# Optimization experiments

Hardware: AMD Instinct MI355X
Metric: run time of the kernel (lower is better)

The kernel has to match this reference:

```python
import jax, jax.numpy as jnp
import numpy as np

B, N, M = 4, 2048, 2048
DIM, DIM_KEYS, DIM_OUT = 512, 512, 512
HEADS, DIM_HEAD = 8, 64
INNER = HEADS * DIM_HEAD


def setup_inputs() -> dict:
    key = jax.random.key(0)
    ks = jax.random.split(key, 9)
    x = jax.random.normal(ks[0], (B, N, DIM), dtype=jnp.float32)
    context = jax.random.normal(ks[1], (B, M, DIM_KEYS), dtype=jnp.float32)
    mask = jax.random.randint(ks[2], (B, N), 0, 2).astype(bool)
    context_mask = jax.random.randint(ks[3], (B, M), 0, 2).astype(bool)
    Wq = jax.random.normal(ks[4], (DIM, INNER), dtype=jnp.float32) * 0.02
    Wkv = jax.random.normal(ks[5], (DIM_KEYS, 2 * INNER), dtype=jnp.float32) * 0.02
    Wo = jax.random.normal(ks[6], (INNER, DIM_OUT), dtype=jnp.float32) * 0.02
    bo = jnp.zeros((DIM_OUT,), dtype=jnp.float32)
    null_key = jax.random.normal(ks[7], (DIM_HEAD,), dtype=jnp.float32)
    null_value = jax.random.normal(ks[8], (DIM_HEAD,), dtype=jnp.float32)
    return {"x": x, "context": context, "mask": mask, "context_mask": context_mask,
            "Wq": Wq, "Wkv": Wkv, "Wo": Wo, "bo": bo,
            "null_key": null_key, "null_value": null_value}


def reference(x, context, mask, context_mask, Wq, Wkv, Wo, bo, null_key, null_value):
    b, n, _ = x.shape
    m = context.shape[1]
    h, dh = HEADS, DIM_HEAD
    scale = dh ** -0.5

    # projections -> [b, h, n, dh]
    q = (x @ Wq).reshape(b, n, h, dh).transpose(0, 2, 1, 3)
    kv = context @ Wkv  # [b, m, 2*inner]
    k, v = jnp.split(kv, 2, axis=-1)
    k = k.reshape(b, m, h, dh).transpose(0, 2, 1, 3)
    v = v.reshape(b, m, h, dh).transpose(0, 2, 1, 3)

    # prepend null key/value token -> j = m + 1
    nk = jnp.broadcast_to(null_key, (b, h, 1, dh))
    nv = jnp.broadcast_to(null_value, (b, h, 1, dh))
    k = jnp.concatenate([nk, k], axis=2)
    v = jnp.concatenate([nv, v], axis=2)

    # qk activation (tanh) BEFORE the dot product
    q = jnp.tanh(q)
    k = jnp.tanh(k)

    sim = jnp.einsum('bhid,bhjd->bhij', q, k) * scale  # [b,h,n,m+1]

    # null token is always attendable -> pad context mask with True
    cm = jnp.pad(context_mask, ((0, 0), (1, 0)), constant_values=True)
    full_mask = mask[:, None, :, None] & cm[:, None, None, :]
    neg = -jnp.finfo(sim.dtype).max
    sim = jnp.where(full_mask, sim, neg)

    attn = jax.nn.softmax(sim, axis=-1)
    out = jnp.einsum('bhij,bhjd->bhid', attn, v)
    out = out.transpose(0, 2, 1, 3).reshape(b, n, h * dh)
    return out @ Wo + bo
```

## Files before the change

### kernel.cpp

```cpp
#include <hip/hip_runtime.h>
#include <math.h>

#define BB 4
#define NN 2048
#define MM 2048
#define HEADS 8
#define DH 64

typedef _Float16 f16;
typedef _Float16 f16x4 __attribute__((ext_vector_type(4)));
typedef _Float16 f16x8 __attribute__((ext_vector_type(8)));
typedef float f32x4 __attribute__((ext_vector_type(4)));
typedef unsigned short ushort;

#define LOG2E 1.44269504088896f
#define QSCALE (0.125f * LOG2E)

#if __has_builtin(__builtin_amdgcn_exp2f)
#define EXP2(x) __builtin_amdgcn_exp2f(x)
#else
#define EXP2(x) exp2f(x)
#endif

__device__ __forceinline__ f16x4 pk4(float a, float b, float c, float d) {
#if __has_builtin(__builtin_amdgcn_cvt_pkrtz)
    auto t0 = __builtin_amdgcn_cvt_pkrtz(a, b);
    auto t1 = __builtin_amdgcn_cvt_pkrtz(c, d);
    f16x4 r;
    r[0] = t0[0]; r[1] = t0[1]; r[2] = t1[0]; r[3] = t1[1];
    return r;
#else
    f16x4 r = {(f16)a, (f16)b, (f16)c, (f16)d};
    return r;
#endif
}

__device__ __forceinline__ void gl16(const void* g, void* l) {
    __builtin_amdgcn_global_load_lds(
        (const __attribute__((address_space(1))) unsigned int*)g,
        (__attribute__((address_space(3))) unsigned int*)l, 16, 0, 0);
}

__global__ void wprep_k(const float* __restrict__ Wq, const float* __restrict__ Wkv,
                        const float* __restrict__ Wo,
                        f16* __restrict__ wq16, f16* __restrict__ wkv16,
                        f16* __restrict__ woh, f16* __restrict__ wol)
{
    __shared__ f16 S0[64 * 36], S1[64 * 36];
    const int tid = threadIdx.x;
    const int bid = blockIdx.x;
    const int K = 512;
    const float* W; int N; f16* T16; f16 *Th, *Tl; int id;
    if (bid < 128)      { W = Wq;  N = 512;  T16 = wq16;  Th = 0; Tl = 0; id = bid; }
    else if (bid < 384) { W = Wkv; N = 1024; T16 = wkv16; Th = 0; Tl = 0; id = bid - 128; }
    else                { W = Wo;  N = 512;  T16 = 0; Th = woh; Tl = wol; id = bid - 384; }
    const int k0 = (id & 15) * 32, n0 = (id >> 4) * 64;
    const int kr = tid >> 3, nc = (tid & 7) * 8;
    float4 v0 = *(const float4*)(W + (size_t)(k0 + kr) * N + n0 + nc);
    float4 v1 = *(const float4*)(W + (size_t)(k0 + kr) * N + n0 + nc + 4);
    float e[8] = {v0.x, v0.y, v0.z, v0.w, v1.x, v1.y, v1.z, v1.w};
    const int n = tid >> 2, kc = (tid & 3) * 8;
    if (T16) {
#pragma unroll
        for (int j = 0; j < 8; j++) S0[(nc + j) * 36 + kr] = (f16)e[j];
        __syncthreads();
        *(uint4*)(T16 + (size_t)(n0 + n) * K + k0 + kc) = *(const uint4*)(S0 + n * 36 + kc);
    } else {
#pragma unroll
        for (int j = 0; j < 8; j++) {
            f16 h = (f16)e[j];
            S0[(nc + j) * 36 + kr] = h;
            S1[(nc + j) * 36 + kr] = (f16)(e[j] - (float)h);
        }
        __syncthreads();
        *(uint4*)(Th + (size_t)(n0 + n) * K + k0 + kc) = *(const uint4*)(S0 + n * 36 + kc);
        *(uint4*)(Tl + (size_t)(n0 + n) * K + k0 + kc) = *(const uint4*)(S1 + n * 36 + kc);
    }
}

__launch_bounds__(256)
__global__ void proj_k(const float* __restrict__ x, const float* __restrict__ ctx,
                       const f16* __restrict__ wq16, const f16* __restrict__ wkv16,
                       f16* __restrict__ qws, f16* __restrict__ kws, f16* __restrict__ vt)
{
    __shared__ f16 sA[128 * 36];
    __shared__ f16 sB[128 * 36];

    const int tid  = threadIdx.x;
    const int wave = tid >> 6, lane = tid & 63;
    const int l15  = lane & 15, quad = lane >> 4;
    const int by = blockIdx.y;
    const int isQ = (by < 4);
    const float* A = isQ ? x : ctx;
    const f16* Bt  = isQ ? wq16 : wkv16;
    const int c0 = (isQ ? by : by - 4) * 128;
    const size_t r0 = (size_t)blockIdx.x * 128;
    const int K = 512;

    const int ar = tid >> 1;
    const int ac = (tid & 1) * 16;

    f32x4 acc[2][8] = {};

    for (int k0 = 0; k0 < K; k0 += 32) {
        const float* ap = A + (r0 + ar) * K + k0 + ac;
        float4 a0 = *(const float4*)(ap + 0);
        float4 a1 = *(const float4*)(ap + 4);
        float4 a2 = *(const float4*)(ap + 8);
        float4 a3 = *(const float4*)(ap + 12);
        uint4 bv0 = *(const uint4*)(Bt + (size_t)(c0 + ar) * K + k0 + ac);
        uint4 bv1 = *(const uint4*)(Bt + (size_t)(c0 + ar) * K + k0 + ac + 8);
        f16x8 pa0, pa1;
        pa0[0] = (f16)a0.x; pa0[1] = (f16)a0.y; pa0[2] = (f16)a0.z; pa0[3] = (f16)a0.w;
        pa0[4] = (f16)a1.x; pa0[5] = (f16)a1.y; pa0[6] = (f16)a1.z; pa0[7] = (f16)a1.w;
        pa1[0] = (f16)a2.x; pa1[1] = (f16)a2.y; pa1[2] = (f16)a2.z; pa1[3] = (f16)a2.w;
        pa1[4] = (f16)a3.x; pa1[5] = (f16)a3.y; pa1[6] = (f16)a3.z; pa1[7] = (f16)a3.w;
        __syncthreads();
        *(f16x8*)(sA + ar * 36 + ac)     = pa0;
        *(f16x8*)(sA + ar * 36 + ac + 8) = pa1;
        *(uint4*)(sB + ar * 36 + ac)     = bv0;
        *(uint4*)(sB + ar * 36 + ac + 8) = bv1;
        __syncthreads();

        f16x8 a[2];
#pragma unroll
        for (int rt = 0; rt < 2; rt++)
            a[rt] = *(const f16x8*)(sA + (wave * 32 + rt * 16 + l15) * 36 + quad * 8);
#pragma unroll
        for (int half = 0; half < 2; half++) {
            f16x8 b[4];
#pragma unroll
            for (int c = 0; c < 4; c++)
                b[c] = *(const f16x8*)(sB + ((half * 4 + c) * 16 + l15) * 36 + quad * 8);
#pragma unroll
            for (int rt = 0; rt < 2; rt++)
#pragma unroll
                for (int c = 0; c < 4; c++)
                    acc[rt][half * 4 + c] = __builtin_amdgcn_mfma_f32_16x16x32_f16(
                        a[rt], b[c], acc[rt][half * 4 + c], 0, 0, 0);
        }
    }

    const int b    = (int)(r0 >> 11);
    const int rloc = ((int)(r0 & 2047)) + wave * 32;

#pragma unroll
    for (int rt = 0; rt < 2; rt++)
#pragma unroll
        for (int ct = 0; ct < 8; ct++) {
            const int col = c0 + ct * 16 + l15;
            if (isQ || col < 512) {
                const int h = (col >> 6) & 7;
                const int d = col & 63;
                f16* dst = isQ ? qws : kws;
                const float sc = isQ ? QSCALE : 1.0f;
#pragma unroll
                for (int reg = 0; reg < 4; reg++) {
                    const int nn = rloc + rt * 16 + quad * 4 + reg;
                    dst[(((size_t)b * 8 + h) * 2048 + nn) * 64 + d] =
                        (f16)(tanhf(acc[rt][ct][reg]) * sc);
                }
            } else {
                const int c = col - 512;
                const int h = c >> 6;
                const int d = c & 63;
                const int m0 = rloc + rt * 16 + quad * 4;
                f16x4 pk;
#pragma unroll
                for (int reg = 0; reg < 4; reg++) pk[reg] = (f16)acc[rt][ct][reg];
                *(f16x4*)(vt + (((size_t)b * 8 + h) * 64 + d) * 2048 + m0) = pk;
            }
        }
}

__launch_bounds__(256, 4)
__global__ void attn_k(const f16* __restrict__ qws, const f16* __restrict__ kws,
                       const f16* __restrict__ vtws,
                       const int* __restrict__ mask, const int* __restrict__ cmask,
                       const float* __restrict__ nk, const float* __restrict__ nv,
                       f16* __restrict__ Opf, float* __restrict__ lp)
{
    __shared__ __align__(16) char smem[32768];

    const int tid  = threadIdx.x;
    const int wave = tid >> 6, lane = tid & 63;
    const int l15  = lane & 15, quad = lane >> 4;
    const int bh = blockIdx.x, b = bh >> 3, h = bh & 7;
    const int q0 = blockIdx.y * 128 + wave * 32;
    const int jh = blockIdx.z;
    const int jbeg = jh << 9, jend = jbeg + 512;

    const f16* kg0 = kws + (size_t)bh * MM * DH;
    const f16* vg0 = vtws + (size_t)bh * DH * MM;

    const int lrow = lane >> 3;
    const int lsw  = ((lane & 7) ^ lrow) << 4;
    const char* kP = (const char*)kg0 + (size_t)(jbeg + wave * 16 + lrow) * 128 + lsw;
    const char* vP = (const char*)vg0 + (size_t)(wave * 16 + lrow) * 4096
                   + (size_t)jbeg * 2 + lsw;
    char* kD = smem + wave * 2048;
    char* vD = smem + 8192 + wave * 2048;

    gl16(kP,         kD);
    gl16(kP + 1024,  kD + 1024);
    gl16(vP,         vD);
    gl16(vP + 32768, vD + 1024);
    kP += 8192; vP += 128;

    f16x8 qf[2][2];
    const f16* qbase = qws + ((size_t)bh * NN + q0) * DH;
#pragma unroll
    for (int rt = 0; rt < 2; rt++)
#pragma unroll
        for (int ks = 0; ks < 2; ks++)
            qf[rt][ks] = *(const f16x8*)(qbase + (rt * 16 + l15) * DH + ks * 32 + quad * 8);

    int rowOk[2];
#pragma unroll
    for (int rt = 0; rt < 2; rt++)
        rowOk[rt] = mask[(size_t)b * NN + q0 + rt * 16 + l15];

    float pnull[2] = {0.0f, 0.0f};
    if (jh == 0) {
        float pn[2] = {0.f, 0.f};
#pragma unroll
        for (int ks = 0; ks < 2; ks++)
#pragma unroll
            for (int t = 0; t < 8; t++) {
                const float nkt = tanhf(nk[ks * 32 + quad * 8 + t]);
                pn[0] += (float)qf[0][ks][t] * nkt;
                pn[1] += (float)qf[1][ks][t] * nkt;
            }
#pragma unroll
        for (int rt = 0; rt < 2; rt++) {
            pn[rt] += __shfl_xor(pn[rt], 16);
            pn[rt] += __shfl_xor(pn[rt], 32);
            pnull[rt] = rowOk[rt] ? EXP2(pn[rt]) : 1.0f;
        }
    }
    float negsel[2];
#pragma unroll
    for (int rt = 0; rt < 2; rt++) {
        negsel[rt] = rowOk[rt] ? -1.0e30f : 0.0f;
        if (!rowOk[rt]) {
            const f16x8 zz = {(f16)0, (f16)0, (f16)0, (f16)0, (f16)0, (f16)0, (f16)0, (f16)0};
            qf[rt][0] = zz; qf[rt][1] = zz;
        }
    }

    f32x4 acc[2][4];
    f32x4 accl[2];
#pragma unroll
    for (int rt = 0; rt < 2; rt++)
#pragma unroll
        for (int reg = 0; reg < 4; reg++) {
            const float pr = __shfl(pnull[rt], quad * 4 + reg, 16);
            accl[rt][reg] = pr;
#pragma unroll
            for (int ds = 0; ds < 4; ds++)
                acc[rt][ds][reg] = pr * nv[ds * 16 + l15];
        }

    const f16x4 vone = {(f16)1, (f16)1, (f16)1, (f16)1};
    const int kxor = l15 & 7;

    __syncthreads();

    int buf = 0;
    for (int jc = jbeg; jc < jend; jc += 64) {
        int4 cmv[4];
#pragma unroll
        for (int jj = 0; jj < 4; jj++)
            cmv[jj] = *(const int4*)(cmask + (size_t)b * MM + jc + jj * 16 + quad * 4);

        if (jc + 64 < jend) {
            const int bo = (buf ^ 1) << 14;
            gl16(kP,         kD + bo);
            gl16(kP + 1024,  kD + bo + 1024);
            gl16(vP,         vD + bo);
            gl16(vP + 32768, vD + bo + 1024);
            kP += 8192; vP += 128;
        }

        const char* sKb = smem + (buf << 14);
        const char* sVb = sKb + 8192;

        f32x4 st[2][4];
#pragma unroll
        for (int rt = 0; rt < 2; rt++)
#pragma unroll
            for (int jj = 0; jj < 4; jj++) {
                st[rt][jj][0] = cmv[jj].x ? 0.0f : negsel[rt];
                st[rt][jj][1] = cmv[jj].y ? 0.0f : negsel[rt];
                st[rt][jj][2] = cmv[jj].z ? 0.0f : negsel[rt];
                st[rt][jj][3] = cmv[jj].w ? 0.0f : negsel[rt];
            }

#pragma unroll
        for (int ks = 0; ks < 2; ks++) {
            f16x8 kb[4];
#pragma unroll
            for (int jj = 0; jj < 4; jj++)
                kb[jj] = *(const f16x8*)(sKb + (jj * 16 + l15) * 128
                                             + (((ks * 4 + quad) ^ kxor) << 4));
#pragma unroll
            for (int rt = 0; rt < 2; rt++)
#pragma unroll
                for (int jj = 0; jj < 4; jj++)
                    st[rt][jj] = __builtin_amdgcn_mfma_f32_16x16x32_f16(
                        kb[jj], qf[rt][ks], st[rt][jj], 0, 0, 0);
        }

        f16x4 pa[2][4];
#pragma unroll
        for (int rt = 0; rt < 2; rt++)
#pragma unroll
            for (int jj = 0; jj < 4; jj++)
                pa[rt][jj] = pk4(EXP2(st[rt][jj][0]), EXP2(st[rt][jj][1]),
                                 EXP2(st[rt][jj][2]), EXP2(st[rt][jj][3]));

#pragma unroll
        for (int jj = 0; jj < 4; jj++) {
            f16x4 vb[4];
#pragma unroll
            for (int ds = 0; ds < 4; ds++)
                vb[ds] = *(const f16x4*)(sVb + (ds * 16 + l15) * 128
                                             + (((jj * 2 + (quad >> 1)) ^ kxor) << 4)
                                             + ((quad & 1) << 3));
#pragma unroll
            for (int rt = 0; rt < 2; rt++) {
#pragma unroll
                for (int ds = 0; ds < 4; ds++)
                    acc[rt][ds] = __builtin_amdgcn_mfma_f32_16x16x16f16(
                        pa[rt][jj], vb[ds], acc[rt][ds], 0, 0, 0);
                accl[rt] = __builtin_amdgcn_mfma_f32_16x16x16f16(
                    pa[rt][jj], vone, accl[rt], 0, 0, 0);
            }
        }

        __syncthreads();
        buf ^= 1;
    }

#pragma unroll
    for (int rt = 0; rt < 2; rt++) {
        float inv[4];
#pragma unroll
        for (int reg = 0; reg < 4; reg++)
            inv[reg] = 1.0f / fmaxf(accl[rt][reg], 1e-35f);
#pragma unroll
        for (int ds = 0; ds < 4; ds++)
#pragma unroll
            for (int reg = 0; reg < 4; reg++) {
                const int r = q0 + rt * 16 + quad * 4 + reg;
                Opf[((size_t)jh * 8192 + b * 2048 + r) * 512 + h * 64 + ds * 16 + l15] =
                    (f16)(acc[rt][ds][reg] * inv[reg]);
            }
    }
    if (l15 == 0) {
#pragma unroll
        for (int rt = 0; rt < 2; rt++)
#pragma unroll
            for (int reg = 0; reg < 4; reg++)
                lp[((size_t)jh * 32 + bh) * 2048 + q0 + rt * 16 + quad * 4 + reg] =
                    accl[rt][reg];
    }
}

__global__ void merge_k(const f16* __restrict__ Opf, const float* __restrict__ lp,
                        f16* __restrict__ of16)
{
    const int i = blockIdx.x * 256 + threadIdx.x;
    const int row = i >> 7;
    const int c4  = i & 127;
    const int b = row >> 11, n = row & 2047, h = c4 >> 4;
    float w[4], den = 0.f;
#pragma unroll
    for (int jh = 0; jh < 4; jh++) {
        w[jh] = lp[((size_t)jh * 32 + b * 8 + h) * 2048 + n];
        den += w[jh];
    }
    const float inv = 1.0f / den;
    float v0 = 0, v1 = 0, v2 = 0, v3 = 0;
#pragma unroll
    for (int jh = 0; jh < 4; jh++) {
        f16x4 o = *(const f16x4*)(Opf + ((size_t)jh * 8192 + row) * 512 + c4 * 4);
        v0 += (float)o[0] * w[jh];
        v1 += (float)o[1] * w[jh];
        v2 += (float)o[2] * w[jh];
        v3 += (float)o[3] * w[jh];
    }
    f16x4 r = pk4(v0 * inv, v1 * inv, v2 * inv, v3 * inv);
    *(f16x4*)(of16 + (size_t)row * 512 + c4 * 4) = r;
}

__launch_bounds__(256)
__global__ void mgemm2(const f16* __restrict__ A, const f16* __restrict__ Bh,
                       const f16* __restrict__ Bl,
                       float* __restrict__ o32, const float* __restrict__ bias,
                       int K)
{
    __shared__ f16 sA[128 * 36];
    __shared__ f16 sBh[64 * 36], sBl[64 * 36];

    const int tid  = threadIdx.x;
    const int wave = tid >> 6, lane = tid & 63;
    const int l15  = lane & 15, quad = lane >> 4;
    const size_t r0 = (size_t)blockIdx.x * 128;
    const int c0 = blockIdx.y * 64;

    const int sr = tid >> 2;
    const int sc = (tid & 3) * 8;

    f32x4 acc[2][4] = {};

    for (int k0 = 0; k0 < K; k0 += 32) {
        uint4 a0 = *(const uint4*)(A + (r0 + sr) * K + k0 + sc);
        uint4 a1 = *(const uint4*)(A + (r0 + 64 + sr) * K + k0 + sc);
        uint4 bh = *(const uint4*)(Bh + (size_t)(c0 + sr) * K + k0 + sc);
        uint4 bl = *(const uint4*)(Bl + (size_t)(c0 + sr) * K + k0 + sc);
        __syncthreads();
        *(uint4*)(sA + sr * 36 + sc)        = a0;
        *(uint4*)(sA + (64 + sr) * 36 + sc) = a1;
        *(uint4*)(sBh + sr * 36 + sc)       = bh;
        *(uint4*)(sBl + sr * 36 + sc)       = bl;
        __syncthreads();

        f16x8 a[2], b_h[4], b_l[4];
#pragma unroll
        for (int rt = 0; rt < 2; rt++)
            a[rt] = *(const f16x8*)(sA + (wave * 32 + rt * 16 + l15) * 36 + quad * 8);
#pragma unroll
        for (int ct = 0; ct < 4; ct++) {
            b_h[ct] = *(const f16x8*)(sBh + (ct * 16 + l15) * 36 + quad * 8);
            b_l[ct] = *(const f16x8*)(sBl + (ct * 16 + l15) * 36 + quad * 8);
        }
#pragma unroll
        for (int rt = 0; rt < 2; rt++)
#pragma unroll
            for (int ct = 0; ct < 4; ct++) {
                acc[rt][ct] = __builtin_amdgcn_mfma_f32_16x16x32_f16(a[rt], b_h[ct], acc[rt][ct], 0, 0, 0);
                acc[rt][ct] = __builtin_amdgcn_mfma_f32_16x16x32_f16(a[rt], b_l[ct], acc[rt][ct], 0, 0, 0);
            }
    }

#pragma unroll
    for (int rt = 0; rt < 2; rt++)
#pragma unroll
        for (int ct = 0; ct < 4; ct++) {
            const int col = c0 + ct * 16 + l15;
            const float bv = bias[col];
#pragma unroll
            for (int reg = 0; reg < 4; reg++) {
                const size_t row = r0 + wave * 32 + rt * 16 + quad * 4 + reg;
                o32[row * 512 + col] = acc[rt][ct][reg] + bv;
            }
        }
}

extern "C" void kernel_launch(void* const* d_in, const int* in_sizes, int n_in,
                              void* d_out, int out_size, void* d_ws, size_t ws_size,
                              hipStream_t stream)
{
    const float* x    = (const float*)d_in[0];
    const float* ctx  = (const float*)d_in[1];
    const int*   mask = (const int*)d_in[2];
    const int*   cmsk = (const int*)d_in[3];
    const float* Wq   = (const float*)d_in[4];
    const float* Wkv  = (const float*)d_in[5];
    const float* Wo   = (const float*)d_in[6];
    const float* bo   = (const float*)d_in[7];
    const float* nk   = (const float*)d_in[8];
    const float* nv   = (const float*)d_in[9];
    float* out = (float*)d_out;

    const size_t S = (size_t)BB * HEADS * NN * DH;

    f16* qws = (f16*)d_ws;
    f16* kws = qws + S;
    f16* vt  = kws + S;
    f16* wq16  = vt + S;
    f16* wkv16 = wq16 + 512 * 512;
    f16* woh = wkv16 + 512 * 1024;
    f16* wol = woh + 512 * 512;
    float* lp = (float*)(wol + 512 * 512);
    f16* Opf = (f16*)(lp + 4 * 32 * 2048);
    f16* of16 = qws;

    wprep_k<<<512, 256, 0, stream>>>(Wq, Wkv, Wo, wq16, wkv16, woh, wol);
    proj_k<<<dim3(64, 12), 256, 0, stream>>>(x, ctx, wq16, wkv16, qws, kws, vt);
    attn_k<<<dim3(32, 16, 4), 256, 0, stream>>>(qws, kws, vt, mask, cmsk, nk, nv, Opf, lp);
    merge_k<<<4096, 256, 0, stream>>>(Opf, lp, of16);
    mgemm2<<<dim3(64, 8), 256, 0, stream>>>(of16, woh, wol, out, bo, 512);
}
```

Before: 201.1 us.

## Pre-convert activations to fp16, precompute mask bias, unroll attention double-buffer loop

A new xprep kernel converts x and context to fp16 once, so the projection GEMM loads half-width A tiles instead of converting fp32 inside every K-step. The context mask becomes a float additive bias in wprep, and attention applies it by multiplying with a per-row float instead of branching on integer selects. The attention loop is manually unrolled into ping-pong tiles with constant buffer offsets, explicit vmcnt waits, a raw barrier and sched_barriers. The extra conversion kernel adds a full read and write of both activations and one more launch, which may cost more than the per-tile conversion work it replaces.

```diff
diff --git a/kernel.cpp b/kernel.cpp
--- a/kernel.cpp
+++ b/kernel.cpp
@@ -42,13 +42,27 @@
 }
 
 __global__ void wprep_k(const float* __restrict__ Wq, const float* __restrict__ Wkv,
-                        const float* __restrict__ Wo,
+                        const float* __restrict__ Wo, const int* __restrict__ cmask,
                         f16* __restrict__ wq16, f16* __restrict__ wkv16,
-                        f16* __restrict__ woh, f16* __restrict__ wol)
+                        f16* __restrict__ woh, f16* __restrict__ wol,
+                        float* __restrict__ cbias)
 {
     __shared__ f16 S0[64 * 36], S1[64 * 36];
     const int tid = threadIdx.x;
     const int bid = blockIdx.x;
+    if (bid >= 512) {
+        const int bb = bid - 512, j0 = tid * 8;
+        int4 m0 = *(const int4*)(cmask + (size_t)bb * MM + j0);
+        int4 m1 = *(const int4*)(cmask + (size_t)bb * MM + j0 + 4);
+        float4 o0, o1;
+        o0.x = m0.x ? 0.f : -1e30f; o0.y = m0.y ? 0.f : -1e30f;
+        o0.z = m0.z ? 0.f : -1e30f; o0.w = m0.w ? 0.f : -1e30f;
+        o1.x = m1.x ? 0.f : -1e30f; o1.y = m1.y ? 0.f : -1e30f;
+        o1.z = m1.z ? 0.f : -1e30f; o1.w = m1.w ? 0.f : -1e30f;
+        *(float4*)(cbias + (size_t)bb * MM + j0)     = o0;
+        *(float4*)(cbias + (size_t)bb * MM + j0 + 4) = o1;
+        return;
+    }
     const int K = 512;
     const float* W; int N; f16* T16; f16 *Th, *Tl; int id;
     if (bid < 128)      { W = Wq;  N = 512;  T16 = wq16;  Th = 0; Tl = 0; id = bid; }
@@ -78,8 +92,23 @@
     }
 }
 
+__global__ void xprep_k(const float* __restrict__ x, const float* __restrict__ ctx,
+                        f16* __restrict__ xf, f16* __restrict__ cf)
+{
+    const size_t S = (size_t)BB * NN * 512;
+    const size_t i = ((size_t)blockIdx.x * 256 + threadIdx.x) * 8;
+    const float* src = (i < S) ? x + i : ctx + (i - S);
+    f16* dst         = (i < S) ? xf + i : cf + (i - S);
+    float4 v0 = *(const float4*)(src);
+    float4 v1 = *(const float4*)(src + 4);
+    f16x8 o;
+    o[0] = (f16)v0.x; o[1] = (f16)v0.y; o[2] = (f16)v0.z; o[3] = (f16)v0.w;
+    o[4] = (f16)v1.x; o[5] = (f16)v1.y; o[6] = (f16)v1.z; o[7] = (f16)v1.w;
+    *(f16x8*)dst = o;
+}
+
 __launch_bounds__(256)
-__global__ void proj_k(const float* __restrict__ x, const float* __restrict__ ctx,
+__global__ void proj_k(const f16* __restrict__ xf, const f16* __restrict__ cf,
                        const f16* __restrict__ wq16, const f16* __restrict__ wkv16,
                        f16* __restrict__ qws, f16* __restrict__ kws, f16* __restrict__ vt)
 {
@@ -91,7 +120,7 @@
     const int l15  = lane & 15, quad = lane >> 4;
     const int by = blockIdx.y;
     const int isQ = (by < 4);
-    const float* A = isQ ? x : ctx;
+    const f16* A16 = isQ ? xf : cf;
     const f16* Bt  = isQ ? wq16 : wkv16;
     const int c0 = (isQ ? by : by - 4) * 128;
     const size_t r0 = (size_t)blockIdx.x * 128;
@@ -103,21 +132,13 @@
     f32x4 acc[2][8] = {};
 
     for (int k0 = 0; k0 < K; k0 += 32) {
-        const float* ap = A + (r0 + ar) * K + k0 + ac;
-        float4 a0 = *(const float4*)(ap + 0);
-        float4 a1 = *(const float4*)(ap + 4);
-        float4 a2 = *(const float4*)(ap + 8);
-        float4 a3 = *(const float4*)(ap + 12);
+        uint4 av0 = *(const uint4*)(A16 + (r0 + ar) * K + k0 + ac);
+        uint4 av1 = *(const uint4*)(A16 + (r0 + ar) * K + k0 + ac + 8);
         uint4 bv0 = *(const uint4*)(Bt + (size_t)(c0 + ar) * K + k0 + ac);
         uint4 bv1 = *(const uint4*)(Bt + (size_t)(c0 + ar) * K + k0 + ac + 8);
-        f16x8 pa0, pa1;
-        pa0[0] = (f16)a0.x; pa0[1] = (f16)a0.y; pa0[2] = (f16)a0.z; pa0[3] = (f16)a0.w;
-        pa0[4] = (f16)a1.x; pa0[5] = (f16)a1.y; pa0[6] = (f16)a1.z; pa0[7] = (f16)a1.w;
-        pa1[0] = (f16)a2.x; pa1[1] = (f16)a2.y; pa1[2] = (f16)a2.z; pa1[3] = (f16)a2.w;
-        pa1[4] = (f16)a3.x; pa1[5] = (f16)a3.y; pa1[6] = (f16)a3.z; pa1[7] = (f16)a3.w;
         __syncthreads();
-        *(f16x8*)(sA + ar * 36 + ac)     = pa0;
-        *(f16x8*)(sA + ar * 36 + ac + 8) = pa1;
+        *(uint4*)(sA + ar * 36 + ac)     = av0;
+        *(uint4*)(sA + ar * 36 + ac + 8) = av1;
         *(uint4*)(sB + ar * 36 + ac)     = bv0;
         *(uint4*)(sB + ar * 36 + ac + 8) = bv1;
         __syncthreads();
@@ -176,7 +197,7 @@
 __launch_bounds__(256, 4)
 __global__ void attn_k(const f16* __restrict__ qws, const f16* __restrict__ kws,
                        const f16* __restrict__ vtws,
-                       const int* __restrict__ mask, const int* __restrict__ cmask,
+                       const int* __restrict__ mask, const float* __restrict__ cbias,
                        const float* __restrict__ nk, const float* __restrict__ nv,
                        f16* __restrict__ Opf, float* __restrict__ lp)
 {
@@ -188,7 +209,7 @@
     const int bh = blockIdx.x, b = bh >> 3, h = bh & 7;
     const int q0 = blockIdx.y * 128 + wave * 32;
     const int jh = blockIdx.z;
-    const int jbeg = jh << 9, jend = jbeg + 512;
+    const int jbeg = jh << 9;
 
     const f16* kg0 = kws + (size_t)bh * MM * DH;
     const f16* vg0 = vtws + (size_t)bh * DH * MM;
@@ -238,10 +259,10 @@
             pnull[rt] = rowOk[rt] ? EXP2(pn[rt]) : 1.0f;
         }
     }
-    float negsel[2];
+    float rowOkf[2];
 #pragma unroll
     for (int rt = 0; rt < 2; rt++) {
-        negsel[rt] = rowOk[rt] ? -1.0e30f : 0.0f;
+        rowOkf[rt] = rowOk[rt] ? 1.0f : 0.0f;
         if (!rowOk[rt]) {
             const f16x8 zz = {(f16)0, (f16)0, (f16)0, (f16)0, (f16)0, (f16)0, (f16)0, (f16)0};
             qf[rt][0] = zz; qf[rt][1] = zz;
@@ -263,84 +284,85 @@
 
     const f16x4 vone = {(f16)1, (f16)1, (f16)1, (f16)1};
     const int kxor = l15 & 7;
-
-    __syncthreads();
-
-    int buf = 0;
-    for (int jc = jbeg; jc < jend; jc += 64) {
-        int4 cmv[4];
-#pragma unroll
-        for (int jj = 0; jj < 4; jj++)
-            cmv[jj] = *(const int4*)(cmask + (size_t)b * MM + jc + jj * 16 + quad * 4);
-
-        if (jc + 64 < jend) {
-            const int bo = (buf ^ 1) << 14;
-            gl16(kP,         kD + bo);
-            gl16(kP + 1024,  kD + bo + 1024);
-            gl16(vP,         vD + bo);
-            gl16(vP + 32768, vD + bo + 1024);
-            kP += 8192; vP += 128;
-        }
-
-        const char* sKb = smem + (buf << 14);
-        const char* sVb = sKb + 8192;
-
-        f32x4 st[2][4];
-#pragma unroll
-        for (int rt = 0; rt < 2; rt++)
-#pragma unroll
-            for (int jj = 0; jj < 4; jj++) {
-                st[rt][jj][0] = cmv[jj].x ? 0.0f : negsel[rt];
-                st[rt][jj][1] = cmv[jj].y ? 0.0f : negsel[rt];
-                st[rt][jj][2] = cmv[jj].z ? 0.0f : negsel[rt];
-                st[rt][jj][3] = cmv[jj].w ? 0.0f : negsel[rt];
-            }
-
-#pragma unroll
-        for (int ks = 0; ks < 2; ks++) {
-            f16x8 kb[4];
-#pragma unroll
-            for (int jj = 0; jj < 4; jj++)
-                kb[jj] = *(const f16x8*)(sKb + (jj * 16 + l15) * 128
-                                             + (((ks * 4 + quad) ^ kxor) << 4));
-#pragma unroll
-            for (int rt = 0; rt < 2; rt++)
-#pragma unroll
-                for (int jj = 0; jj < 4; jj++)
-                    st[rt][jj] = __builtin_amdgcn_mfma_f32_16x16x32_f16(
-                        kb[jj], qf[rt][ks], st[rt][jj], 0, 0, 0);
-        }
-
-        f16x4 pa[2][4];
-#pragma unroll
-        for (int rt = 0; rt < 2; rt++)
-#pragma unroll
-            for (int jj = 0; jj < 4; jj++)
-                pa[rt][jj] = pk4(EXP2(st[rt][jj][0]), EXP2(st[rt][jj][1]),
-                                 EXP2(st[rt][jj][2]), EXP2(st[rt][jj][3]));
-
-#pragma unroll
-        for (int jj = 0; jj < 4; jj++) {
-            f16x4 vb[4];
-#pragma unroll
-            for (int ds = 0; ds < 4; ds++)
-                vb[ds] = *(const f16x4*)(sVb + (ds * 16 + l15) * 128
-                                             + (((jj * 2 + (quad >> 1)) ^ kxor) << 4)
-                                             + ((quad & 1) << 3));
-#pragma unroll
-            for (int rt = 0; rt < 2; rt++) {
-#pragma unroll
-                for (int ds = 0; ds < 4; ds++)
-                    acc[rt][ds] = __builtin_amdgcn_mfma_f32_16x16x16f16(
-                        pa[rt][jj], vb[ds], acc[rt][ds], 0, 0, 0);
-                accl[rt] = __builtin_amdgcn_mfma_f32_16x16x16f16(
-                    pa[rt][jj], vone, accl[rt], 0, 0, 0);
-            }
-        }
-
-        __syncthreads();
-        buf ^= 1;
-    }
+    const float* cbb = cbias + (size_t)b * MM;
+
+#define ATTN_TILE(BUF, NXT, JC, PF)                                           \
+  {                                                                           \
+    asm volatile("s_waitcnt vmcnt(0)" ::: "memory");                          \
+    __builtin_amdgcn_s_barrier();                                             \
+    __builtin_amdgcn_sched_barrier(0);                                        \
+    float4 cbv[4];                                                            \
+    _Pragma("unroll")                                                         \
+    for (int jj = 0; jj < 4; jj++)                                            \
+      cbv[jj] = *(const float4*)(cbb + (JC) + jj * 16 + quad * 4);            \
+    __builtin_amdgcn_sched_barrier(0);                                        \
+    if (PF) {                                                                 \
+      gl16(kP,         kD + (NXT));                                           \
+      gl16(kP + 1024,  kD + (NXT) + 1024);                                    \
+      gl16(vP,         vD + (NXT));                                           \
+      gl16(vP + 32768, vD + (NXT) + 1024);                                    \
+      kP += 8192; vP += 128;                                                  \
+    }                                                                         \
+    __builtin_amdgcn_sched_barrier(0);                                        \
+    const char* sKb = smem + (BUF);                                           \
+    const char* sVb = smem + (BUF) + 8192;                                    \
+    f32x4 st[2][4];                                                           \
+    _Pragma("unroll")                                                         \
+    for (int rt = 0; rt < 2; rt++)                                            \
+      _Pragma("unroll")                                                       \
+      for (int jj = 0; jj < 4; jj++)                                          \
+        _Pragma("unroll")                                                     \
+        for (int reg = 0; reg < 4; reg++)                                     \
+          st[rt][jj][reg] = cbv[jj][reg] * rowOkf[rt];                        \
+    _Pragma("unroll")                                                         \
+    for (int ks = 0; ks < 2; ks++) {                                          \
+      f16x8 kb[4];                                                            \
+      _Pragma("unroll")                                                       \
+      for (int jj = 0; jj < 4; jj++)                                          \
+        kb[jj] = *(const f16x8*)(sKb + (jj * 16 + l15) * 128                  \
+                                     + (((ks * 4 + quad) ^ kxor) << 4));      \
+      _Pragma("unroll")                                                       \
+      for (int rt = 0; rt < 2; rt++)                                          \
+        _Pragma("unroll")                                                     \
+        for (int jj = 0; jj < 4; jj++)                                        \
+          st[rt][jj] = __builtin_amdgcn_mfma_f32_16x16x32_f16(                \
+              kb[jj], qf[rt][ks], st[rt][jj], 0, 0, 0);                       \
+    }                                                                         \
+    f16x4 pa[2][4];                                                           \
+    _Pragma("unroll")                                                         \
+    for (int rt = 0; rt < 2; rt++)                                            \
+      _Pragma("unroll")                                                       \
+      for (int jj = 0; jj < 4; jj++)                                          \
+        pa[rt][jj] = pk4(EXP2(st[rt][jj][0]), EXP2(st[rt][jj][1]),            \
+                         EXP2(st[rt][jj][2]), EXP2(st[rt][jj][3]));           \
+    _Pragma("unroll")                                                         \
+    for (int jj = 0; jj < 4; jj++) {                                          \
+      f16x4 vb[4];                                                            \
+      _Pragma("unroll")                                                       \
+      for (int ds = 0; ds < 4; ds++)                                          \
+        vb[ds] = *(const f16x4*)(sVb + (ds * 16 + l15) * 128                  \
+                                     + (((jj * 2 + (quad >> 1)) ^ kxor) << 4) \
+                                     + ((quad & 1) << 3));                    \
+      _Pragma("unroll")                                                       \
+      for (int rt = 0; rt < 2; rt++) {                                        \
+        _Pragma("unroll")                                                     \
+        for (int ds = 0; ds < 4; ds++)                                        \
+          acc[rt][ds] = __builtin_amdgcn_mfma_f32_16x16x16f16(                \
+              pa[rt][jj], vb[ds], acc[rt][ds], 0, 0, 0);                      \
+        accl[rt] = __builtin_amdgcn_mfma_f32_16x16x16f16(                     \
+            pa[rt][jj], vone, accl[rt], 0, 0, 0);                             \
+      }                                                                       \
+    }                                                                         \
+  }
+
+    int jc = jbeg;
+    for (int it = 0; it < 4; it++) {
+        ATTN_TILE(0,     16384, jc, 1);
+        jc += 64;
+        ATTN_TILE(16384, 0,     jc, it < 3);
+        jc += 64;
+    }
+#undef ATTN_TILE
 
 #pragma unroll
     for (int rt = 0; rt < 2; rt++) {
@@ -486,10 +508,14 @@
     float* lp = (float*)(wol + 512 * 512);
     f16* Opf = (f16*)(lp + 4 * 32 * 2048);
     f16* of16 = qws;
-
-    wprep_k<<<512, 256, 0, stream>>>(Wq, Wkv, Wo, wq16, wkv16, woh, wol);
-    proj_k<<<dim3(64, 12), 256, 0, stream>>>(x, ctx, wq16, wkv16, qws, kws, vt);
-    attn_k<<<dim3(32, 16, 4), 256, 0, stream>>>(qws, kws, vt, mask, cmsk, nk, nv, Opf, lp);
+    f16* xf16 = Opf;
+    f16* cf16 = xf16 + (size_t)BB * NN * 512;
+    float* cbias = (float*)(Opf + (size_t)4 * 8192 * 512);
+
+    wprep_k<<<516, 256, 0, stream>>>(Wq, Wkv, Wo, cmsk, wq16, wkv16, woh, wol, cbias);
+    xprep_k<<<4096, 256, 0, stream>>>(x, ctx, xf16, cf16);
+    proj_k<<<dim3(64, 12), 256, 0, stream>>>(xf16, cf16, wq16, wkv16, qws, kws, vt);
+    attn_k<<<dim3(32, 16, 4), 256, 0, stream>>>(qws, kws, vt, mask, cbias, nk, nv, Opf, lp);
     merge_k<<<4096, 256, 0, stream>>>(Opf, lp, of16);
     mgemm2<<<dim3(64, 8), 256, 0, stream>>>(of16, woh, wol, out, bo, 512);
 }
```

After: 205.8 us. +2.3%, slower.

## Double-buffer projection and output GEMMs with async global-to-LDS loads

Applied to the files above, without the earlier changes.

Adds a pre-pass kernel that converts x and context to fp16 so the projection GEMM can stream fp16 tiles. Both the projection GEMM and the output GEMM now use double-buffered LDS filled by direct global-to-LDS loads (gl16) with an XOR swizzle instead of padding. The output GEMM tile widens from 64 to 128 columns. This targets global-load latency and register staging in the GEMM main loops, at the cost of an extra kernel launch and an extra round trip through memory for the converted activations.

```diff
diff --git a/kernel.cpp b/kernel.cpp
--- a/kernel.cpp
+++ b/kernel.cpp
@@ -78,60 +78,79 @@
     }
 }
 
-__launch_bounds__(256)
-__global__ void proj_k(const float* __restrict__ x, const float* __restrict__ ctx,
+__global__ void xprep_k(const float* __restrict__ x, const float* __restrict__ ctx,
+                        f16* __restrict__ xf, f16* __restrict__ cf)
+{
+    const size_t S = (size_t)BB * NN * 512;
+    const size_t i = ((size_t)blockIdx.x * 256 + threadIdx.x) * 8;
+    const float* src = (i < S) ? x + i : ctx + (i - S);
+    f16* dst         = (i < S) ? xf + i : cf + (i - S);
+    float4 v0 = *(const float4*)(src);
+    float4 v1 = *(const float4*)(src + 4);
+    f16x8 o;
+    o[0] = (f16)v0.x; o[1] = (f16)v0.y; o[2] = (f16)v0.z; o[3] = (f16)v0.w;
+    o[4] = (f16)v1.x; o[5] = (f16)v1.y; o[6] = (f16)v1.z; o[7] = (f16)v1.w;
+    *(f16x8*)dst = o;
+}
+
+__launch_bounds__(256, 3)
+__global__ void proj_k(const f16* __restrict__ xf, const f16* __restrict__ cf,
                        const f16* __restrict__ wq16, const f16* __restrict__ wkv16,
                        f16* __restrict__ qws, f16* __restrict__ kws, f16* __restrict__ vt)
 {
-    __shared__ f16 sA[128 * 36];
-    __shared__ f16 sB[128 * 36];
+    __shared__ __align__(16) char smem[32768];
 
     const int tid  = threadIdx.x;
     const int wave = tid >> 6, lane = tid & 63;
     const int l15  = lane & 15, quad = lane >> 4;
     const int by = blockIdx.y;
     const int isQ = (by < 4);
-    const float* A = isQ ? x : ctx;
+    const f16* A16 = isQ ? xf : cf;
     const f16* Bt  = isQ ? wq16 : wkv16;
     const int c0 = (isQ ? by : by - 4) * 128;
     const size_t r0 = (size_t)blockIdx.x * 128;
     const int K = 512;
 
-    const int ar = tid >> 1;
-    const int ac = (tid & 1) * 16;
+    const int row0 = wave * 32 + (lane >> 2);
+    const int swc  = (lane & 3) ^ ((lane >> 3) & 3);
+    const char* aP0 = (const char*)(A16 + (r0 + row0) * K)       + swc * 16;
+    const char* aP1 = (const char*)(A16 + (r0 + row0 + 16) * K)  + swc * 16;
+    const char* bP0 = (const char*)(Bt + (size_t)(c0 + row0) * K)      + swc * 16;
+    const char* bP1 = (const char*)(Bt + (size_t)(c0 + row0 + 16) * K) + swc * 16;
+    char* aD = smem + wave * 2048;
+    char* bD = smem + 8192 + wave * 2048;
+
+    gl16(aP0, aD); gl16(aP1, aD + 1024);
+    gl16(bP0, bD); gl16(bP1, bD + 1024);
+    aP0 += 64; aP1 += 64; bP0 += 64; bP1 += 64;
+
+    const int fsw = ((quad ^ ((l15 >> 1) & 3)) << 4);
+    const int aoff0 = (wave * 32 + l15) * 64 + fsw;
+    const int aoff1 = (wave * 32 + 16 + l15) * 64 + fsw;
 
     f32x4 acc[2][8] = {};
-
-    for (int k0 = 0; k0 < K; k0 += 32) {
-        const float* ap = A + (r0 + ar) * K + k0 + ac;
-        float4 a0 = *(const float4*)(ap + 0);
-        float4 a1 = *(const float4*)(ap + 4);
-        float4 a2 = *(const float4*)(ap + 8);
-        float4 a3 = *(const float4*)(ap + 12);
-        uint4 bv0 = *(const uint4*)(Bt + (size_t)(c0 + ar) * K + k0 + ac);
-        uint4 bv1 = *(const uint4*)(Bt + (size_t)(c0 + ar) * K + k0 + ac + 8);
-        f16x8 pa0, pa1;
-        pa0[0] = (f16)a0.x; pa0[1] = (f16)a0.y; pa0[2] = (f16)a0.z; pa0[3] = (f16)a0.w;
-        pa0[4] = (f16)a1.x; pa0[5] = (f16)a1.y; pa0[6] = (f16)a1.z; pa0[7] = (f16)a1.w;
-        pa1[0] = (f16)a2.x; pa1[1] = (f16)a2.y; pa1[2] = (f16)a2.z; pa1[3] = (f16)a2.w;
-        pa1[4] = (f16)a3.x; pa1[5] = (f16)a3.y; pa1[6] = (f16)a3.z; pa1[7] = (f16)a3.w;
-        __syncthreads();
-        *(f16x8*)(sA + ar * 36 + ac)     = pa0;
-        *(f16x8*)(sA + ar * 36 + ac + 8) = pa1;
-        *(uint4*)(sB + ar * 36 + ac)     = bv0;
-        *(uint4*)(sB + ar * 36 + ac + 8) = bv1;
-        __syncthreads();
+    __syncthreads();
+
+    int buf = 0;
+    for (int t = 0; t < 16; t++) {
+        const int nb = (buf ^ 1) * 16384;
+        if (t < 15) {
+            gl16(aP0, aD + nb); gl16(aP1, aD + nb + 1024);
+            gl16(bP0, bD + nb); gl16(bP1, bD + nb + 1024);
+            aP0 += 64; aP1 += 64; bP0 += 64; bP1 += 64;
+        }
+        const char* sA = smem + buf * 16384;
+        const char* sB = sA + 8192;
 
         f16x8 a[2];
-#pragma unroll
-        for (int rt = 0; rt < 2; rt++)
-            a[rt] = *(const f16x8*)(sA + (wave * 32 + rt * 16 + l15) * 36 + quad * 8);
+        a[0] = *(const f16x8*)(sA + aoff0);
+        a[1] = *(const f16x8*)(sA + aoff1);
 #pragma unroll
         for (int half = 0; half < 2; half++) {
             f16x8 b[4];
 #pragma unroll
             for (int c = 0; c < 4; c++)
-                b[c] = *(const f16x8*)(sB + ((half * 4 + c) * 16 + l15) * 36 + quad * 8);
+                b[c] = *(const f16x8*)(sB + ((half * 4 + c) * 16 + l15) * 64 + fsw);
 #pragma unroll
             for (int rt = 0; rt < 2; rt++)
 #pragma unroll
@@ -139,6 +158,8 @@
                     acc[rt][half * 4 + c] = __builtin_amdgcn_mfma_f32_16x16x32_f16(
                         a[rt], b[c], acc[rt][half * 4 + c], 0, 0, 0);
         }
+        __syncthreads();
+        buf ^= 1;
     }
 
     const int b    = (int)(r0 >> 11);
@@ -394,60 +415,86 @@
     *(f16x4*)(of16 + (size_t)row * 512 + c4 * 4) = r;
 }
 
-__launch_bounds__(256)
+__launch_bounds__(256, 3)
 __global__ void mgemm2(const f16* __restrict__ A, const f16* __restrict__ Bh,
                        const f16* __restrict__ Bl,
                        float* __restrict__ o32, const float* __restrict__ bias,
                        int K)
 {
-    __shared__ f16 sA[128 * 36];
-    __shared__ f16 sBh[64 * 36], sBl[64 * 36];
+    __shared__ __align__(16) char smem[49152];
 
     const int tid  = threadIdx.x;
     const int wave = tid >> 6, lane = tid & 63;
     const int l15  = lane & 15, quad = lane >> 4;
     const size_t r0 = (size_t)blockIdx.x * 128;
-    const int c0 = blockIdx.y * 64;
-
-    const int sr = tid >> 2;
-    const int sc = (tid & 3) * 8;
-
-    f32x4 acc[2][4] = {};
-
-    for (int k0 = 0; k0 < K; k0 += 32) {
-        uint4 a0 = *(const uint4*)(A + (r0 + sr) * K + k0 + sc);
-        uint4 a1 = *(const uint4*)(A + (r0 + 64 + sr) * K + k0 + sc);
-        uint4 bh = *(const uint4*)(Bh + (size_t)(c0 + sr) * K + k0 + sc);
-        uint4 bl = *(const uint4*)(Bl + (size_t)(c0 + sr) * K + k0 + sc);
+    const int c0 = blockIdx.y * 128;
+
+    const int row0 = wave * 32 + (lane >> 2);
+    const int swc  = (lane & 3) ^ ((lane >> 3) & 3);
+    const char* aP0 = (const char*)(A + (r0 + row0) * K)       + swc * 16;
+    const char* aP1 = (const char*)(A + (r0 + row0 + 16) * K)  + swc * 16;
+    const char* hP0 = (const char*)(Bh + (size_t)(c0 + row0) * K)      + swc * 16;
+    const char* hP1 = (const char*)(Bh + (size_t)(c0 + row0 + 16) * K) + swc * 16;
+    const char* lP0 = (const char*)(Bl + (size_t)(c0 + row0) * K)      + swc * 16;
+    const char* lP1 = (const char*)(Bl + (size_t)(c0 + row0 + 16) * K) + swc * 16;
+    char* aD = smem + wave * 2048;
+    char* hD = smem + 8192 + wave * 2048;
+    char* lD = smem + 16384 + wave * 2048;
+
+    gl16(aP0, aD); gl16(aP1, aD + 1024);
+    gl16(hP0, hD); gl16(hP1, hD + 1024);
+    gl16(lP0, lD); gl16(lP1, lD + 1024);
+    aP0 += 64; aP1 += 64; hP0 += 64; hP1 += 64; lP0 += 64; lP1 += 64;
+
+    const int fsw = ((quad ^ ((l15 >> 1) & 3)) << 4);
+    const int aoff0 = (wave * 32 + l15) * 64 + fsw;
+    const int aoff1 = (wave * 32 + 16 + l15) * 64 + fsw;
+
+    f32x4 acc[2][8] = {};
+    __syncthreads();
+
+    int buf = 0;
+    const int NT = K / 32;
+    for (int t = 0; t < NT; t++) {
+        const int nb = (buf ^ 1) * 24576;
+        if (t < NT - 1) {
+            gl16(aP0, aD + nb); gl16(aP1, aD + nb + 1024);
+            gl16(hP0, hD + nb); gl16(hP1, hD + nb + 1024);
+            gl16(lP0, lD + nb); gl16(lP1, lD + nb + 1024);
+            aP0 += 64; aP1 += 64; hP0 += 64; hP1 += 64; lP0 += 64; lP1 += 64;
+        }
+        const char* sA = smem + buf * 24576;
+        const char* sH = sA + 8192;
+        const char* sL = sA + 16384;
+
+        f16x8 a[2];
+        a[0] = *(const f16x8*)(sA + aoff0);
+        a[1] = *(const f16x8*)(sA + aoff1);
+#pragma unroll
+        for (int half = 0; half < 2; half++) {
+#pragma unroll
+            for (int c = 0; c < 4; c++) {
+                const int ct = half * 4 + c;
+                const int boff = (ct * 16 + l15) * 64 + fsw;
+                f16x8 bh = *(const f16x8*)(sH + boff);
+                f16x8 bl = *(const f16x8*)(sL + boff);
+#pragma unroll
+                for (int rt = 0; rt < 2; rt++) {
+                    acc[rt][ct] = __builtin_amdgcn_mfma_f32_16x16x32_f16(
+                        a[rt], bh, acc[rt][ct], 0, 0, 0);
+                    acc[rt][ct] = __builtin_amdgcn_mfma_f32_16x16x32_f16(
+                        a[rt], bl, acc[rt][ct], 0, 0, 0);
+                }
+            }
+        }
         __syncthreads();
-        *(uint4*)(sA + sr * 36 + sc)        = a0;
-        *(uint4*)(sA + (64 + sr) * 36 + sc) = a1;
-        *(uint4*)(sBh + sr * 36 + sc)       = bh;
-        *(uint4*)(sBl + sr * 36 + sc)       = bl;
-        __syncthreads();
-
-        f16x8 a[2], b_h[4], b_l[4];
-#pragma unroll
-        for (int rt = 0; rt < 2; rt++)
-            a[rt] = *(const f16x8*)(sA + (wave * 32 + rt * 16 + l15) * 36 + quad * 8);
-#pragma unroll
-        for (int ct = 0; ct < 4; ct++) {
-            b_h[ct] = *(const f16x8*)(sBh + (ct * 16 + l15) * 36 + quad * 8);
-            b_l[ct] = *(const f16x8*)(sBl + (ct * 16 + l15) * 36 + quad * 8);
-        }
-#pragma unroll
-        for (int rt = 0; rt < 2; rt++)
-#pragma unroll
-            for (int ct = 0; ct < 4; ct++) {
-                acc[rt][ct] = __builtin_amdgcn_mfma_f32_16x16x32_f16(a[rt], b_h[ct], acc[rt][ct], 0, 0, 0);
-                acc[rt][ct] = __builtin_amdgcn_mfma_f32_16x16x32_f16(a[rt], b_l[ct], acc[rt][ct], 0, 0, 0);
-            }
+        buf ^= 1;
     }
 
 #pragma unroll
     for (int rt = 0; rt < 2; rt++)
 #pragma unroll
-        for (int ct = 0; ct < 4; ct++) {
+        for (int ct = 0; ct < 8; ct++) {
             const int col = c0 + ct * 16 + l15;
             const float bv = bias[col];
 #pragma unroll
@@ -486,10 +533,13 @@
     float* lp = (float*)(wol + 512 * 512);
     f16* Opf = (f16*)(lp + 4 * 32 * 2048);
     f16* of16 = qws;
+    f16* xf16 = Opf;
+    f16* cf16 = xf16 + (size_t)BB * NN * 512;
 
     wprep_k<<<512, 256, 0, stream>>>(Wq, Wkv, Wo, wq16, wkv16, woh, wol);
-    proj_k<<<dim3(64, 12), 256, 0, stream>>>(x, ctx, wq16, wkv16, qws, kws, vt);
+    xprep_k<<<4096, 256, 0, stream>>>(x, ctx, xf16, cf16);
+    proj_k<<<dim3(64, 12), 256, 0, stream>>>(xf16, cf16, wq16, wkv16, qws, kws, vt);
     attn_k<<<dim3(32, 16, 4), 256, 0, stream>>>(qws, kws, vt, mask, cmsk, nk, nv, Opf, lp);
     merge_k<<<4096, 256, 0, stream>>>(Opf, lp, of16);
-    mgemm2<<<dim3(64, 8), 256, 0, stream>>>(of16, woh, wol, out, bo, 512);
-}
+    mgemm2<<<dim3(64, 4), 256, 0, stream>>>(of16, woh, wol, out, bo, 512);
+}
```

Measured after the change: 199.2 us. Within noise of the previous version (-0.9%).
